# Optimization experiments

Hardware: AMD Instinct MI355X
Metric: run time of the kernel (lower is better)

## Reference

```python
import jax, jax.numpy as jnp
import numpy as np


def _gather_corner(flat_feats, iz, iy, ix, H, W, B, F, Hg, Wg):
    # flat_feats: [B, F, D*H*W]; iz/iy/ix: [B, Hg, Wg] int32 (already clamped)
    lin = (iz * H + iy) * W + ix                      # [B, Hg, Wg]
    lin = jnp.broadcast_to(lin.reshape(B, 1, Hg * Wg), (B, F, Hg * Wg))
    return jnp.take_along_axis(flat_feats, lin, axis=2).reshape(B, F, Hg, Wg)


def setup_inputs() -> dict:
    key = jax.random.key(0)
    k1, k2 = jax.random.split(key)
    input_feats = jax.random.normal(k1, (4, 8, 128, 128, 128), dtype=jnp.float32)
    sampling_grid = jax.random.normal(k2, (4, 512, 512, 3), dtype=jnp.float32)
    return {"input_feats": input_feats, "sampling_grid": sampling_grid}


def reference(input_feats, sampling_grid):
    B, F, D, H, W = input_feats.shape
    Hg, Wg = sampling_grid.shape[1], sampling_grid.shape[2]

    # map grid from [-1,1] to voxel coordinates [0, dim-1]
    g = jnp.clip(sampling_grid, -1.0, 1.0)
    scale = jnp.array([W - 1.0, H - 1.0, D - 1.0], dtype=sampling_grid.dtype)
    g = (g + 1.0) * 0.5 * scale                      # [B, Hg, Wg, 3] in x,y,z order
    x, y, z = g[..., 0], g[..., 1], g[..., 2]

    x0 = jnp.floor(x); y0 = jnp.floor(y); z0 = jnp.floor(z)
    u = (x - x0)[:, None]                            # [B,1,Hg,Wg]
    v = (y - y0)[:, None]
    w = (z - z0)[:, None]

    # nearest grid_sample with align_corners=True on integer coords == clamped index
    def clampi(a, hi):
        return jnp.clip(a, 0, hi).astype(jnp.int32)

    ix0 = clampi(x0, W - 1); ix1 = clampi(x0 + 1.0, W - 1)
    iy0 = clampi(y0, H - 1); iy1 = clampi(y0 + 1.0, H - 1)
    iz0 = clampi(z0, D - 1); iz1 = clampi(z0 + 1.0, D - 1)

    flat = input_feats.reshape(B, F, D * H * W)
    gc = lambda iz, iy, ix: _gather_corner(flat, iz, iy, ix, H, W, B, F, Hg, Wg)

    c000 = gc(iz0, iy0, ix0); c001 = gc(iz1, iy0, ix0)
    c010 = gc(iz0, iy1, ix0); c011 = gc(iz1, iy1, ix0)
    c100 = gc(iz0, iy0, ix1); c101 = gc(iz1, iy0, ix1)
    c110 = gc(iz0, iy1, ix1); c111 = gc(iz1, iy1, ix1)

    out = ((1 - u) * (1 - v) * (1 - w) * c000 + (1 - u) * (1 - v) * w * c001
           + (1 - u) * v * (1 - w) * c010 + (1 - u) * v * w * c011
           + u * (1 - v) * (1 - w) * c100 + u * (1 - v) * w * c101
           + u * v * (1 - w) * c110 + u * v * w * c111)
    return out  # [B, F, Hg, Wg]
```

## Files before the change

### kernel.cpp

```cpp
#include <hip/hip_runtime.h>
#include <hip/hip_fp16.h>


#define NB 4
#define NF 8
#define ND 128
#define NH 128
#define NW 128
#define HG 512
#define WG 512

#define PTOT (HG * WG)
#define TOTAL (NB * PTOT)
#define NBINS_C (NB * 32)
#define HBLK 512
#define SPB (TOTAL / HBLK)

typedef float        __attribute__((ext_vector_type(4))) f32x4;
typedef unsigned int __attribute__((ext_vector_type(4))) u32x4;

__global__ __launch_bounds__(256) void transform_kernel(
    const float* __restrict__ feats, __half* __restrict__ T)
{
    const size_t S = (size_t)ND * NH * NW;
    size_t tid = (size_t)blockIdx.x * blockDim.x + threadIdx.x;
    size_t b  = tid / (S / 4);
    size_t s4 = (tid - b * (S / 4)) * 4;

    const float* fb = feats + b * NF * S;
    __half* tb = T + (b * S + s4) * NF;

    f32x4 vals[NF];
#pragma unroll
    for (int f = 0; f < NF; ++f)
        vals[f] = __builtin_nontemporal_load(
            (const f32x4*)(fb + (size_t)f * S + s4));

#pragma unroll
    for (int i = 0; i < 4; ++i) {
        u32x4 hv;
#pragma unroll
        for (int f = 0; f < 4; ++f) {
            __half2 h = __floats2half2_rn(vals[2 * f][i], vals[2 * f + 1][i]);
            hv[f] = *(const unsigned*)&h;
        }
        *(u32x4*)(tb + (size_t)i * NF) = hv;
    }
}

__device__ __forceinline__ void grid_to_voxel(
    const float* __restrict__ g, float& x, float& y, float& z)
{
    x = __builtin_nontemporal_load(g + 0);
    y = __builtin_nontemporal_load(g + 1);
    z = __builtin_nontemporal_load(g + 2);
    x = fminf(fmaxf(x, -1.0f), 1.0f);
    y = fminf(fmaxf(y, -1.0f), 1.0f);
    z = fminf(fmaxf(z, -1.0f), 1.0f);
    x = (x + 1.0f) * 0.5f * (float)(NW - 1);
    y = (y + 1.0f) * 0.5f * (float)(NH - 1);
    z = (z + 1.0f) * 0.5f * (float)(ND - 1);
}

__device__ __forceinline__ int sample_bin(int idx, float z)
{
    int iz0 = min(max((int)floorf(z), 0), ND - 1);
    return ((idx >> 18) << 5) | (iz0 >> 2);
}

__global__ __launch_bounds__(256) void hist_kernel(
    const float* __restrict__ grid, unsigned* __restrict__ counts)
{
    __shared__ unsigned h[NBINS_C];
    int t = threadIdx.x, blk = blockIdx.x;
    if (t < NBINS_C) h[t] = 0u;
    __syncthreads();
#pragma unroll
    for (int k = 0; k < SPB / 256; ++k) {
        int idx = blk * SPB + k * 256 + t;
        float x, y, z;
        grid_to_voxel(grid + (size_t)idx * 3, x, y, z);
        atomicAdd(&h[sample_bin(idx, z)], 1u);
    }
    __syncthreads();
    if (t < NBINS_C) counts[(size_t)t * HBLK + blk] = h[t];
}

__global__ __launch_bounds__(128) void scan_kernel(unsigned* __restrict__ counts)
{
    __shared__ unsigned tot[NBINS_C];
    int t = threadIdx.x;
    unsigned s = 0;
    for (int k = 0; k < HBLK; ++k) s += counts[(size_t)t * HBLK + k];
    tot[t] = s;
    __syncthreads();
    for (int off = 1; off < NBINS_C; off <<= 1) {
        unsigned add = (t >= off) ? tot[t - off] : 0u;
        __syncthreads();
        tot[t] += add;
        __syncthreads();
    }
    unsigned run = (t == 0) ? 0u : tot[t - 1];
    for (int k = 0; k < HBLK; ++k) {
        unsigned c = counts[(size_t)t * HBLK + k];
        counts[(size_t)t * HBLK + k] = run;
        run += c;
    }
}

__global__ __launch_bounds__(256) void scatter_kernel(
    const float* __restrict__ grid, const unsigned* __restrict__ counts,
    u32x4* __restrict__ payload)
{
    __shared__ unsigned cur[NBINS_C];
    int t = threadIdx.x, blk = blockIdx.x;
    if (t < NBINS_C) cur[t] = counts[(size_t)t * HBLK + blk];
    __syncthreads();
#pragma unroll
    for (int k = 0; k < SPB / 256; ++k) {
        int idx = blk * SPB + k * 256 + t;
        float x, y, z;
        grid_to_voxel(grid + (size_t)idx * 3, x, y, z);
        int bin = sample_bin(idx, z);
        unsigned slot = atomicAdd(&cur[bin], 1u);
        u32x4 pl;
        pl.x = __float_as_uint(x);
        pl.y = __float_as_uint(y);
        pl.z = __float_as_uint(z);
        pl.w = (unsigned)idx;
        payload[slot] = pl;
    }
}

__device__ __forceinline__ void pair_accum(
    const u32x4& lov, const u32x4& hiv, bool hi,
    float wr, float um, float u, float acc[NF])
{
    u32x4 c0 = hi ? hiv : lov;
    const u32x4& c1 = hiv;
#pragma unroll
    for (int j = 0; j < 4; ++j) {
        unsigned u0 = c0[j], u1 = c1[j];
        float2 f0 = __half22float2(*(const __half2*)&u0);
        float2 f1 = __half22float2(*(const __half2*)&u1);
        acc[2 * j]     = fmaf(wr, fmaf(u, f1.x, um * f0.x), acc[2 * j]);
        acc[2 * j + 1] = fmaf(wr, fmaf(u, f1.y, um * f0.y), acc[2 * j + 1]);
    }
}

__global__ __launch_bounds__(256) void gather_kernel(
    const __half* __restrict__ T, const u32x4* __restrict__ payload,
    float* __restrict__ outT)
{
    int bid = blockIdx.x;
    int chunk = (bid & 7) * ((TOTAL / 256) / 8) + (bid >> 3);
    int slot = chunk * 256 + threadIdx.x;

    u32x4 pl = payload[slot];
    float x = __uint_as_float(pl.x);
    float y = __uint_as_float(pl.y);
    float z = __uint_as_float(pl.z);
    int b = (int)(pl.w >> 18);

    float xf = floorf(x), yf = floorf(y), zf = floorf(z);
    float u = x - xf, v = y - yf, w = z - zf;
    float um = 1.0f - u, vm = 1.0f - v, wm = 1.0f - w;

    int ix0 = min(max((int)xf, 0), NW - 1);
    int iy0 = min(max((int)yf, 0), NH - 1);
    int iy1 = min(iy0 + 1, NH - 1);
    int iz0 = min(max((int)zf, 0), ND - 1);
    int iz1 = min(iz0 + 1, ND - 1);

    int xb = min(ix0, NW - 2);
    bool hi = (ix0 != xb);

    const __half* tb = T + (size_t)b * ((size_t)ND * NH * NW) * NF;
    size_t r00 = ((size_t)(iz0 * NH + iy0) * NW + xb) * NF;
    size_t r01 = ((size_t)(iz0 * NH + iy1) * NW + xb) * NF;
    size_t r10 = ((size_t)(iz1 * NH + iy0) * NW + xb) * NF;
    size_t r11 = ((size_t)(iz1 * NH + iy1) * NW + xb) * NF;

    u32x4 L[8];
    L[0] = *(const u32x4*)(tb + r00);
    L[1] = *(const u32x4*)(tb + r00 + NF);
    L[2] = *(const u32x4*)(tb + r01);
    L[3] = *(const u32x4*)(tb + r01 + NF);
    L[4] = *(const u32x4*)(tb + r10);
    L[5] = *(const u32x4*)(tb + r10 + NF);
    L[6] = *(const u32x4*)(tb + r11);
    L[7] = *(const u32x4*)(tb + r11 + NF);

    float acc[NF];
#pragma unroll
    for (int f = 0; f < NF; ++f) acc[f] = 0.0f;

    pair_accum(L[0], L[1], hi, wm * vm, um, u, acc);
    pair_accum(L[2], L[3], hi, wm * v,  um, u, acc);
    pair_accum(L[4], L[5], hi, w  * vm, um, u, acc);
    pair_accum(L[6], L[7], hi, w  * v,  um, u, acc);

    float* op = outT + (size_t)pl.w * NF;
    f32x4 o0, o1;
#pragma unroll
    for (int j = 0; j < 4; ++j) { o0[j] = acc[j]; o1[j] = acc[4 + j]; }
    *(f32x4*)op       = o0;
    *(f32x4*)(op + 4) = o1;
}

__global__ __launch_bounds__(256) void finalize_kernel(
    const float* __restrict__ outT, float* __restrict__ out)
{
    int i = blockIdx.x * blockDim.x + threadIdx.x;
    const f32x4* ip = (const f32x4*)(outT + (size_t)i * NF);
    f32x4 a = ip[0];
    f32x4 c = ip[1];
    int b = i >> 18;
    int p = i & (PTOT - 1);
    float* o = out + (size_t)b * NF * PTOT + p;
#pragma unroll
    for (int j = 0; j < 4; ++j) {
        __builtin_nontemporal_store(a[j], o + (size_t)j * PTOT);
        __builtin_nontemporal_store(c[j], o + (size_t)(4 + j) * PTOT);
    }
}

__global__ __launch_bounds__(256) void trilerp_half_kernel(
    const __half* __restrict__ T,
    const float* __restrict__ grid,
    float* __restrict__ out)
{
    const int P = HG * WG;
    int idx = blockIdx.x * blockDim.x + threadIdx.x;
    int b = idx >> 18;
    int p = idx & (P - 1);

    float x, y, z;
    grid_to_voxel(grid + (size_t)idx * 3, x, y, z);

    float xf = floorf(x), yf = floorf(y), zf = floorf(z);
    float u = x - xf, v = y - yf, w = z - zf;
    float um = 1.0f - u, vm = 1.0f - v, wm = 1.0f - w;

    int ix0 = min(max((int)xf, 0), NW - 1);
    int iy0 = min(max((int)yf, 0), NH - 1);
    int iy1 = min(iy0 + 1, NH - 1);
    int iz0 = min(max((int)zf, 0), ND - 1);
    int iz1 = min(iz0 + 1, ND - 1);

    int xb = min(ix0, NW - 2);
    bool hi = (ix0 != xb);

    const __half* tb = T + (size_t)b * ((size_t)ND * NH * NW) * NF;
    size_t r00 = ((size_t)(iz0 * NH + iy0) * NW + xb) * NF;
    size_t r01 = ((size_t)(iz0 * NH + iy1) * NW + xb) * NF;
    size_t r10 = ((size_t)(iz1 * NH + iy0) * NW + xb) * NF;
    size_t r11 = ((size_t)(iz1 * NH + iy1) * NW + xb) * NF;

    u32x4 L[8];
    L[0] = *(const u32x4*)(tb + r00);
    L[1] = *(const u32x4*)(tb + r00 + NF);
    L[2] = *(const u32x4*)(tb + r01);
    L[3] = *(const u32x4*)(tb + r01 + NF);
    L[4] = *(const u32x4*)(tb + r10);
    L[5] = *(const u32x4*)(tb + r10 + NF);
    L[6] = *(const u32x4*)(tb + r11);
    L[7] = *(const u32x4*)(tb + r11 + NF);

    float acc[NF];
#pragma unroll
    for (int f = 0; f < NF; ++f) acc[f] = 0.0f;

    pair_accum(L[0], L[1], hi, wm * vm, um, u, acc);
    pair_accum(L[2], L[3], hi, wm * v,  um, u, acc);
    pair_accum(L[4], L[5], hi, w  * vm, um, u, acc);
    pair_accum(L[6], L[7], hi, w  * v,  um, u, acc);

    float* o = out + (size_t)b * NF * P + p;
#pragma unroll
    for (int f = 0; f < NF; ++f)
        __builtin_nontemporal_store(acc[f], o + (size_t)f * P);
}

__global__ __launch_bounds__(256) void trilerp_f32_kernel(
    const float* __restrict__ feats,
    const float* __restrict__ grid,
    float* __restrict__ out)
{
    const int P = HG * WG;
    int idx = blockIdx.x * blockDim.x + threadIdx.x;
    int b = idx >> 18;
    int p = idx & (P - 1);

    const float* g = grid + (size_t)idx * 3;
    float x = g[0], y = g[1], z = g[2];
    x = fminf(fmaxf(x, -1.0f), 1.0f);
    y = fminf(fmaxf(y, -1.0f), 1.0f);
    z = fminf(fmaxf(z, -1.0f), 1.0f);
    x = (x + 1.0f) * 0.5f * (float)(NW - 1);
    y = (y + 1.0f) * 0.5f * (float)(NH - 1);
    z = (z + 1.0f) * 0.5f * (float)(ND - 1);

    float xf = floorf(x), yf = floorf(y), zf = floorf(z);
    float u = x - xf, v = y - yf, w = z - zf;

    int ix0 = min(max((int)xf, 0), NW - 1);
    int ix1 = min(ix0 + 1, NW - 1);
    int iy0 = min(max((int)yf, 0), NH - 1);
    int iy1 = min(iy0 + 1, NH - 1);
    int iz0 = min(max((int)zf, 0), ND - 1);
    int iz1 = min(iz0 + 1, ND - 1);

    float um = 1.0f - u, vm = 1.0f - v, wm = 1.0f - w;
    float w000 = um * vm * wm, w100 = u * vm * wm;
    float w010 = um * v * wm,  w110 = u * v * wm;
    float w001 = um * vm * w,  w101 = u * vm * w;
    float w011 = um * v * w,   w111 = u * v * w;

    int off00 = (iz0 * NH + iy0) * NW;
    int off01 = (iz0 * NH + iy1) * NW;
    int off10 = (iz1 * NH + iy0) * NW;
    int off11 = (iz1 * NH + iy1) * NW;

    const size_t fstride = (size_t)ND * NH * NW;
    const float* fb = feats + (size_t)b * NF * fstride;
    float* o = out + (size_t)b * NF * P + p;

#pragma unroll
    for (int f = 0; f < NF; ++f) {
        const float* fp = fb + (size_t)f * fstride;
        float r = w000 * fp[off00 + ix0] + w100 * fp[off00 + ix1]
                + w010 * fp[off01 + ix0] + w110 * fp[off01 + ix1]
                + w001 * fp[off10 + ix0] + w101 * fp[off10 + ix1]
                + w011 * fp[off11 + ix0] + w111 * fp[off11 + ix1];
        o[(size_t)f * P] = r;
    }
}

extern "C" void kernel_launch(void* const* d_in, const int* in_sizes, int n_in,
                              void* d_out, int out_size, void* d_ws, size_t ws_size,
                              hipStream_t stream) {
    const float* feats = (const float*)d_in[0];
    const float* grid  = (const float*)d_in[1];
    float* out = (float*)d_out;

    const size_t T_BYTES   = (size_t)NB * ND * NH * NW * NF * sizeof(__half);
    const size_t OFF_PAYL  = T_BYTES;
    const size_t OFF_OUTT  = OFF_PAYL + (size_t)TOTAL * 16;
    const size_t OFF_CNT   = OFF_OUTT + (size_t)TOTAL * NF * sizeof(float);
    const size_t NEED_FULL = OFF_CNT + (size_t)NBINS_C * HBLK * sizeof(unsigned);

    if (ws_size >= NEED_FULL) {
        char* ws = (char*)d_ws;
        __half*   T       = (__half*)ws;
        u32x4*    payload = (u32x4*)(ws + OFF_PAYL);
        float*    outT    = (float*)(ws + OFF_OUTT);
        unsigned* counts  = (unsigned*)(ws + OFF_CNT);

        const int tthreads = NB * ND * NH * NW / 4;
        transform_kernel<<<tthreads / 256, 256, 0, stream>>>(feats, T);

        hist_kernel<<<HBLK, 256, 0, stream>>>(grid, counts);
        scan_kernel<<<1, 128, 0, stream>>>(counts);
        scatter_kernel<<<HBLK, 256, 0, stream>>>(grid, counts, payload);
        gather_kernel<<<TOTAL / 256, 256, 0, stream>>>(T, payload, outT);
        finalize_kernel<<<TOTAL / 256, 256, 0, stream>>>(outT, out);
    } else if (ws_size >= T_BYTES) {
        __half* T = (__half*)d_ws;
        const int tthreads = NB * ND * NH * NW / 4;
        transform_kernel<<<tthreads / 256, 256, 0, stream>>>(feats, T);
        const int total = NB * HG * WG;
        trilerp_half_kernel<<<total / 256, 256, 0, stream>>>(T, grid, out);
    } else {
        const int total = NB * HG * WG;
        trilerp_f32_kernel<<<total / 256, 256, 0, stream>>>(feats, grid, out);
    }
}
```

Before: 483.8 us.

## Parallelize bin prefix scan across blocks and use nontemporal loads in finalize

Replaces the single-block serial exclusive scan over per-block bin counts with a two-level scan. One block per bin scans its block counts in parallel, a small kernel scans the bin totals, and scatter adds the bin base when initializing its cursors. This targets the long serial loop in the single-workgroup scan kernel. The finalize kernel also reads the staged output with nontemporal loads to avoid polluting cache. It adds one extra kernel launch and two small workspace arrays.

Result: faster. 463.1 us (-4.3%).

```diff
diff --git a/kernel.cpp b/kernel.cpp
--- a/kernel.cpp
+++ b/kernel.cpp
@@ -86,35 +86,51 @@
     if (t < NBINS_C) counts[(size_t)t * HBLK + blk] = h[t];
 }
 
-__global__ __launch_bounds__(128) void scan_kernel(unsigned* __restrict__ counts)
-{
-    __shared__ unsigned tot[NBINS_C];
+__global__ __launch_bounds__(256) void scanA_kernel(
+    unsigned* __restrict__ counts, unsigned* __restrict__ binTot)
+{
+    __shared__ unsigned s[256];
+    int b = blockIdx.x, t = threadIdx.x;
+    unsigned c0 = counts[(size_t)b * HBLK + 2 * t];
+    unsigned c1 = counts[(size_t)b * HBLK + 2 * t + 1];
+    s[t] = c0 + c1;
+    __syncthreads();
+    for (int off = 1; off < 256; off <<= 1) {
+        unsigned add = (t >= off) ? s[t - off] : 0u;
+        __syncthreads();
+        s[t] += add;
+        __syncthreads();
+    }
+    unsigned ex = (t == 0) ? 0u : s[t - 1];
+    counts[(size_t)b * HBLK + 2 * t]     = ex;
+    counts[(size_t)b * HBLK + 2 * t + 1] = ex + c0;
+    if (t == 255) binTot[b] = s[255];
+}
+
+__global__ __launch_bounds__(128) void scanB_kernel(
+    const unsigned* __restrict__ binTot, unsigned* __restrict__ binBase)
+{
+    __shared__ unsigned s[NBINS_C];
     int t = threadIdx.x;
-    unsigned s = 0;
-    for (int k = 0; k < HBLK; ++k) s += counts[(size_t)t * HBLK + k];
-    tot[t] = s;
+    s[t] = binTot[t];
     __syncthreads();
     for (int off = 1; off < NBINS_C; off <<= 1) {
-        unsigned add = (t >= off) ? tot[t - off] : 0u;
+        unsigned add = (t >= off) ? s[t - off] : 0u;
         __syncthreads();
-        tot[t] += add;
+        s[t] += add;
         __syncthreads();
     }
-    unsigned run = (t == 0) ? 0u : tot[t - 1];
-    for (int k = 0; k < HBLK; ++k) {
-        unsigned c = counts[(size_t)t * HBLK + k];
-        counts[(size_t)t * HBLK + k] = run;
-        run += c;
-    }
+    binBase[t] = (t == 0) ? 0u : s[t - 1];
 }
 
 __global__ __launch_bounds__(256) void scatter_kernel(
     const float* __restrict__ grid, const unsigned* __restrict__ counts,
-    u32x4* __restrict__ payload)
+    const unsigned* __restrict__ binBase, u32x4* __restrict__ payload)
 {
     __shared__ unsigned cur[NBINS_C];
     int t = threadIdx.x, blk = blockIdx.x;
-    if (t < NBINS_C) cur[t] = counts[(size_t)t * HBLK + blk];
+    if (t < NBINS_C)
+        cur[t] = binBase[t] + counts[(size_t)t * HBLK + blk];
     __syncthreads();
 #pragma unroll
     for (int k = 0; k < SPB / 256; ++k) {
@@ -212,9 +228,8 @@
     const float* __restrict__ outT, float* __restrict__ out)
 {
     int i = blockIdx.x * blockDim.x + threadIdx.x;
-    const f32x4* ip = (const f32x4*)(outT + (size_t)i * NF);
-    f32x4 a = ip[0];
-    f32x4 c = ip[1];
+    f32x4 a = __builtin_nontemporal_load((const f32x4*)(outT + (size_t)i * NF));
+    f32x4 c = __builtin_nontemporal_load((const f32x4*)(outT + (size_t)i * NF) + 1);
     int b = i >> 18;
     int p = i & (PTOT - 1);
     float* o = out + (size_t)b * NF * PTOT + p;
@@ -348,7 +363,9 @@
     const size_t OFF_PAYL  = T_BYTES;
     const size_t OFF_OUTT  = OFF_PAYL + (size_t)TOTAL * 16;
     const size_t OFF_CNT   = OFF_OUTT + (size_t)TOTAL * NF * sizeof(float);
-    const size_t NEED_FULL = OFF_CNT + (size_t)NBINS_C * HBLK * sizeof(unsigned);
+    const size_t OFF_BTOT  = OFF_CNT + (size_t)NBINS_C * HBLK * sizeof(unsigned);
+    const size_t OFF_BBASE = OFF_BTOT + (size_t)NBINS_C * sizeof(unsigned);
+    const size_t NEED_FULL = OFF_BBASE + (size_t)NBINS_C * sizeof(unsigned);
 
     if (ws_size >= NEED_FULL) {
         char* ws = (char*)d_ws;
@@ -356,13 +373,16 @@
         u32x4*    payload = (u32x4*)(ws + OFF_PAYL);
         float*    outT    = (float*)(ws + OFF_OUTT);
         unsigned* counts  = (unsigned*)(ws + OFF_CNT);
+        unsigned* binTot  = (unsigned*)(ws + OFF_BTOT);
+        unsigned* binBase = (unsigned*)(ws + OFF_BBASE);
 
         const int tthreads = NB * ND * NH * NW / 4;
         transform_kernel<<<tthreads / 256, 256, 0, stream>>>(feats, T);
 
         hist_kernel<<<HBLK, 256, 0, stream>>>(grid, counts);
-        scan_kernel<<<1, 128, 0, stream>>>(counts);
-        scatter_kernel<<<HBLK, 256, 0, stream>>>(grid, counts, payload);
+        scanA_kernel<<<NBINS_C, 256, 0, stream>>>(counts, binTot);
+        scanB_kernel<<<1, NBINS_C, 0, stream>>>(binTot, binBase);
+        scatter_kernel<<<HBLK, 256, 0, stream>>>(grid, counts, binBase, payload);
         gather_kernel<<<TOTAL / 256, 256, 0, stream>>>(T, payload, outT);
         finalize_kernel<<<TOTAL / 256, 256, 0, stream>>>(outT, out);
     } else if (ws_size >= T_BYTES) {
```
